# Kernel optimization log

Hardware: AMD Instinct MI355X
Metric: run time of the kernel (lower is better)

Reference implementation:

```python
import jax, jax.numpy as jnp
import numpy as np

NUM_CAMS, BS, NUM_QUERY, MAX_LEN, EMBED_DIMS, NPTS = 6, 1, 40000, 10000, 256, 4


def setup_inputs() -> dict:
    key = jax.random.key(0)
    kq, kr, km = jax.random.split(key, 3)
    query = jax.random.normal(kq, (BS, NUM_QUERY, EMBED_DIMS), dtype=jnp.float32)
    reference_points_cam = jax.random.normal(
        kr, (NUM_CAMS, BS, NUM_QUERY, NPTS, 2), dtype=jnp.float32)
    bev_mask = jax.random.randint(km, (NUM_CAMS, BS, NUM_QUERY, NPTS), 0, 2).astype(jnp.int32)
    return {"query": query, "reference_points_cam": reference_points_cam, "bev_mask": bev_mask}


def reference(query, reference_points_cam, bev_mask):
    # valid[c, q]: query q is seen by camera c (any of the NPTS mask bits set); bs == 1
    valid = (bev_mask > 0).any(-1)            # (cams, bs, Q) bool
    valid0 = valid[:, 0]                      # (cams, Q)

    # Stable stream compaction: valid indices first, in ascending query order.
    order = jnp.argsort(~valid0, axis=-1, stable=True)      # (cams, Q)
    indexes = order[:, :MAX_LEN].astype(jnp.int32)          # (cams, max_len)
    indexes_len = jnp.minimum(valid0.sum(-1), MAX_LEN).astype(jnp.int32)  # (cams,)

    # Padded gather/rebatch; zero out slots beyond each camera's valid count.
    pos_ok = jnp.arange(MAX_LEN)[None, :] < indexes_len[:, None]          # (cams, max_len)
    queries_rebatch = query[0][indexes]                                   # (cams, max_len, E)
    queries_rebatch = jnp.where(pos_ok[:, :, None], queries_rebatch, 0.0)

    ref0 = reference_points_cam[:, 0]                                     # (cams, Q, NPTS, 2)
    reference_points_rebatch = jax.vmap(lambda r, i: r[i])(ref0, indexes) # (cams, max_len, NPTS, 2)
    reference_points_rebatch = jnp.where(
        pos_ok[:, :, None, None], reference_points_rebatch, 0.0)

    # count_norm: 1 / (number of cameras that see each query, clamped to >= 1)
    count = valid.astype(jnp.float32).sum(0)                 # (bs, Q)
    count_norm = (1.0 / jnp.maximum(count, 1.0))[..., None]  # (bs, Q, 1)

    return (indexes,
            indexes_len,
            queries_rebatch.reshape(BS * NUM_CAMS, MAX_LEN, EMBED_DIMS),
            reference_points_rebatch.reshape(BS * NUM_CAMS, MAX_LEN, NPTS, 2),
            count_norm)
```

## Files before the change

### kernel.cpp

```cpp
#include <hip/hip_runtime.h>
#include <hip/hip_bf16.h>

#define NUM_CAMS 6
#define NQ       40000
#define MAX_LEN  10000
#define ED       256
#define NBLK     ((NQ + 255) / 256)

typedef float f32x2 __attribute__((ext_vector_type(2)));

#define OFF_IDX  0
#define OFF_LEN  (NUM_CAMS * MAX_LEN)
#define OFF_Q    (OFF_LEN + NUM_CAMS)
#define OFF_REF  (OFF_Q + NUM_CAMS * MAX_LEN * ED)
#define OFF_CNT  (OFF_REF + NUM_CAMS * MAX_LEN * 8)

#define WS_OFF 0
#define WS_LEN (NUM_CAMS * NBLK)
#define WS_POS (WS_LEN + NUM_CAMS + 4)
#define WS_NEED_BYTES ((WS_POS + NUM_CAMS * NQ) * 4)

#define QBLOCKS      (NQ / 4)
#define TAIL_BLOCKS  (NUM_CAMS * MAX_LEN / 4)
#define CNT_BLOCKS   ((NQ + 255) / 256)
#define GATHER_BLOCKS (NUM_CAMS * MAX_LEN / 4)

__global__ void kA_counts(const int* __restrict__ bev, float* __restrict__ out,
                          int* __restrict__ ws) {
    __shared__ int cnt[NUM_CAMS];
    const int tid = threadIdx.x;
    const int blk = blockIdx.x;
    const int q   = blk * 256 + tid;
    if (tid < NUM_CAMS) cnt[tid] = 0;
    __syncthreads();
    const int lane = tid & 63;
    const bool inb = q < NQ;
    int myCount = 0;
    #pragma unroll
    for (int cam = 0; cam < NUM_CAMS; ++cam) {
        bool v = false;
        if (inb) {
            const int4 m = *reinterpret_cast<const int4*>(bev + ((size_t)cam * NQ + q) * 4);
            v = (m.x > 0) | (m.y > 0) | (m.z > 0) | (m.w > 0);
        }
        myCount += v ? 1 : 0;
        unsigned long long bal = __ballot(v);
        if (lane == 0) atomicAdd(&cnt[cam], __popcll(bal));
    }
    if (inb) out[OFF_CNT + q] = 1.0f / fmaxf((float)myCount, 1.0f);
    __syncthreads();
    if (tid < NUM_CAMS) ws[WS_OFF + tid * NBLK + blk] = cnt[tid];
}

__global__ void kBC_indexes(const int* __restrict__ bev, float* __restrict__ out,
                            int* __restrict__ ws, int usePos) {
    const int blk = blockIdx.x;
    const int cam = blockIdx.y;
    const int tid = threadIdx.x;
    const int lane = tid & 63;
    const int wave = tid >> 6;

    const int part = (tid < NBLK) ? ws[WS_OFF + cam * NBLK + tid] : 0;
    int t = part;
    int o = (tid < blk) ? part : 0;
    #pragma unroll
    for (int d = 1; d < 64; d <<= 1) {
        t += __shfl_xor(t, d, 64);
        o += __shfl_xor(o, d, 64);
    }
    __shared__ int sT[4], sO[4];
    if (lane == 0) { sT[wave] = t; sO[wave] = o; }
    __syncthreads();
    const int total    = sT[0] + sT[1] + sT[2] + sT[3];
    const int blockOff = sO[0] + sO[1] + sO[2] + sO[3];

    if (blk == 0 && tid == 0) {
        const int len = total < MAX_LEN ? total : MAX_LEN;
        ws[WS_LEN + cam] = len;
        out[OFF_LEN + cam] = (float)len;
    }

    const int q   = blk * 256 + tid;
    const bool inb = q < NQ;
    bool v = false;
    if (inb) {
        const int4 m = *reinterpret_cast<const int4*>(bev + ((size_t)cam * NQ + q) * 4);
        v = (m.x > 0) | (m.y > 0) | (m.z > 0) | (m.w > 0);
    }
    const unsigned long long bal = __ballot(v);
    __shared__ int waveSums[4];
    if (lane == 0) waveSums[wave] = __popcll(bal);
    __syncthreads();
    int waveOff = 0;
    #pragma unroll
    for (int w = 0; w < 4; ++w)
        if (w < wave) waveOff += waveSums[w];
    const int prefix = __popcll(bal & ((1ull << lane) - 1ull));
    if (inb) {
        const int vb  = blockOff + waveOff + prefix;
        const int pos = v ? vb : (total + (q - vb));
        if (pos < MAX_LEN) out[OFF_IDX + cam * MAX_LEN + pos] = (float)q;
        if (usePos) ws[WS_POS + cam * NQ + q] = (v && vb < MAX_LEN) ? vb : -1;
    }
}

__global__ void kGatherQ(const float* __restrict__ query, const float* __restrict__ refp,
                         float* __restrict__ out, const int* __restrict__ ws) {
    const int blk   = blockIdx.x;
    const int tid   = threadIdx.x;
    const int group = tid >> 6;
    const int lane  = tid & 63;
    if (blk >= QBLOCKS) {
        const int rowId = (blk - QBLOCKS) * 4 + group;
        const int cam   = rowId / MAX_LEN;
        const int j     = rowId - cam * MAX_LEN;
        if (j < ws[WS_LEN + cam]) return;
        const f32x2 z = (f32x2)(0.f);
        f32x2* o2 = reinterpret_cast<f32x2*>(out + OFF_Q + (size_t)rowId * ED + lane * 4);
        o2[0] = z; o2[1] = z;
        if (lane < 4)
            *reinterpret_cast<f32x2*>(out + OFF_REF + (size_t)rowId * 8 + lane * 2) = z;
        return;
    }
    const int q = blk * 4 + group;

    int pos[NUM_CAMS];
    bool any = false;
    #pragma unroll
    for (int cam = 0; cam < NUM_CAMS; ++cam) {
        const int p = ws[WS_POS + cam * NQ + q];
        pos[cam] = p;
        any |= (p >= 0);
    }
    if (!any) return;

    const float4 vq = *reinterpret_cast<const float4*>(query + (size_t)q * ED + lane * 4);
    f32x2 a; a.x = vq.x; a.y = vq.y;
    f32x2 b; b.x = vq.z; b.y = vq.w;

    #pragma unroll
    for (int cam = 0; cam < NUM_CAMS; ++cam) {
        const int p = pos[cam];
        if (p >= 0) {
            f32x2* o2 = reinterpret_cast<f32x2*>(out + OFF_Q + ((size_t)cam * MAX_LEN + p) * ED + lane * 4);
            o2[0] = a;
            o2[1] = b;
            if (lane < 4) {
                const f32x2 r = *reinterpret_cast<const f32x2*>(refp + ((size_t)cam * NQ + q) * 8 + lane * 2);
                *reinterpret_cast<f32x2*>(out + OFF_REF + ((size_t)cam * MAX_LEN + p) * 8 + lane * 2) = r;
            }
        }
    }
}

__global__ void kGather(const float* __restrict__ query, const float* __restrict__ refp,
                        float* __restrict__ out, const int* __restrict__ ws,
                        const int* __restrict__ bev) {
    const int blk = blockIdx.x;
    const int tid = threadIdx.x;
    if (blk >= GATHER_BLOCKS) {
        const int q = (blk - GATHER_BLOCKS) * 256 + tid;
        if (q < NQ) {
            int cnt = 0;
            #pragma unroll
            for (int cam = 0; cam < NUM_CAMS; ++cam) {
                const int4 m = *reinterpret_cast<const int4*>(bev + ((size_t)cam * NQ + q) * 4);
                cnt += ((m.x > 0) | (m.y > 0) | (m.z > 0) | (m.w > 0)) ? 1 : 0;
            }
            out[OFF_CNT + q] = 1.0f / fmaxf((float)cnt, 1.0f);
        }
        return;
    }
    const int rowId = blk * 4 + (tid >> 6);
    const int lane  = tid & 63;
    const int cam   = rowId / MAX_LEN;
    const int j     = rowId - cam * MAX_LEN;
    const int len   = ws[WS_LEN + cam];

    f32x2 a = (f32x2)(0.f), b = (f32x2)(0.f), r0 = (f32x2)(0.f), r1 = (f32x2)(0.f);
    if (j < len) {
        const int idx = (int)out[OFF_IDX + cam * MAX_LEN + j];
        const float4 vq = *reinterpret_cast<const float4*>(query + (size_t)idx * ED + lane * 4);
        a.x = vq.x; a.y = vq.y;
        b.x = vq.z; b.y = vq.w;
        if (lane < 2) {
            const float4 r = *reinterpret_cast<const float4*>(refp + ((size_t)cam * NQ + idx) * 8 + lane * 4);
            r0.x = r.x; r0.y = r.y;
            r1.x = r.z; r1.y = r.w;
        }
    }
    f32x2* o2 = reinterpret_cast<f32x2*>(out + OFF_Q + (size_t)rowId * ED + lane * 4);
    o2[0] = a;
    o2[1] = b;
    if (lane < 2) {
        f32x2* r2 = reinterpret_cast<f32x2*>(out + OFF_REF + (size_t)rowId * 8 + lane * 4);
        r2[0] = r0;
        r2[1] = r1;
    }
}

extern "C" void kernel_launch(void* const* d_in, const int* in_sizes, int n_in,
                              void* d_out, int out_size, void* d_ws, size_t ws_size,
                              hipStream_t stream) {
    const float* query = (const float*)d_in[0];
    const float* refp  = (const float*)d_in[1];
    const int*   bev   = (const int*)d_in[2];
    float* out = (float*)d_out;
    int*   ws  = (int*)d_ws;
    const int usePos = (ws_size >= (size_t)WS_NEED_BYTES) ? 1 : 0;

    kA_counts<<<NBLK, 256, 0, stream>>>(bev, out, ws);
    kBC_indexes<<<dim3(NBLK, NUM_CAMS), 256, 0, stream>>>(bev, out, ws, usePos);
    if (usePos) {
        kGatherQ<<<QBLOCKS + TAIL_BLOCKS, 256, 0, stream>>>(query, refp, out, ws);
    } else {
        kGather<<<GATHER_BLOCKS + CNT_BLOCKS, 256, 0, stream>>>(query, refp, out, ws, bev);
    }
}
```

Measured before the change: 31.20 us.

## Cache per-wave validity ballots in workspace and use grid-stride gather

The counting kernel now stores each wave's 64-bit validity ballot in workspace, so the index kernel reads one mask per wave instead of reloading the mask tensor and re-ballotting. The gather kernel switches from one block per work item (about 25k blocks) to a fixed 2048-block grid-stride loop. This is meant to cut redundant mask-tensor reads and block launch/scheduling overhead. In exchange it adds workspace writes and makes each block work serially through several items, which may lower memory-level parallelism.

Measured after the change: 30.99 us (median of 2 runs). No clear change (-0.7%).

```diff
diff --git a/kernel.cpp b/kernel.cpp
--- a/kernel.cpp
+++ b/kernel.cpp
@@ -15,18 +15,21 @@
 #define OFF_REF  (OFF_Q + NUM_CAMS * MAX_LEN * ED)
 #define OFF_CNT  (OFF_REF + NUM_CAMS * MAX_LEN * 8)
 
-#define WS_OFF 0
-#define WS_LEN (NUM_CAMS * NBLK)
-#define WS_POS (WS_LEN + NUM_CAMS + 4)
+#define WS_OFF    0
+#define WS_MASK_I 960
+#define WS_MASK_N (NUM_CAMS * NBLK * 4)
+#define WS_LEN    (WS_MASK_I + 2 * WS_MASK_N)
+#define WS_POS    (WS_LEN + 8)
 #define WS_NEED_BYTES ((WS_POS + NUM_CAMS * NQ) * 4)
 
 #define QBLOCKS      (NQ / 4)
 #define TAIL_BLOCKS  (NUM_CAMS * MAX_LEN / 4)
+#define GATHER_GRID  2048
 #define CNT_BLOCKS   ((NQ + 255) / 256)
 #define GATHER_BLOCKS (NUM_CAMS * MAX_LEN / 4)
 
 __global__ void kA_counts(const int* __restrict__ bev, float* __restrict__ out,
-                          int* __restrict__ ws) {
+                          int* __restrict__ ws, int usePos) {
     __shared__ int cnt[NUM_CAMS];
     const int tid = threadIdx.x;
     const int blk = blockIdx.x;
@@ -34,7 +37,9 @@
     if (tid < NUM_CAMS) cnt[tid] = 0;
     __syncthreads();
     const int lane = tid & 63;
+    const int wave = tid >> 6;
     const bool inb = q < NQ;
+    unsigned long long* wsm = reinterpret_cast<unsigned long long*>(ws + WS_MASK_I);
     int myCount = 0;
     #pragma unroll
     for (int cam = 0; cam < NUM_CAMS; ++cam) {
@@ -44,8 +49,11 @@
             v = (m.x > 0) | (m.y > 0) | (m.z > 0) | (m.w > 0);
         }
         myCount += v ? 1 : 0;
-        unsigned long long bal = __ballot(v);
-        if (lane == 0) atomicAdd(&cnt[cam], __popcll(bal));
+        const unsigned long long bal = __ballot(v);
+        if (lane == 0) {
+            atomicAdd(&cnt[cam], __popcll(bal));
+            if (usePos) wsm[((size_t)cam * NBLK + blk) * 4 + wave] = bal;
+        }
     }
     if (inb) out[OFF_CNT + q] = 1.0f / fmaxf((float)myCount, 1.0f);
     __syncthreads();
@@ -68,8 +76,23 @@
         t += __shfl_xor(t, d, 64);
         o += __shfl_xor(o, d, 64);
     }
-    __shared__ int sT[4], sO[4];
-    if (lane == 0) { sT[wave] = t; sO[wave] = o; }
+    __shared__ int sT[4], sO[4], waveSums[4];
+
+    unsigned long long mask;
+    if (usePos) {
+        const unsigned long long* wsm =
+            reinterpret_cast<const unsigned long long*>(ws + WS_MASK_I);
+        mask = wsm[((size_t)cam * NBLK + blk) * 4 + wave];
+    } else {
+        const int q = blk * 256 + tid;
+        bool v = false;
+        if (q < NQ) {
+            const int4 m = *reinterpret_cast<const int4*>(bev + ((size_t)cam * NQ + q) * 4);
+            v = (m.x > 0) | (m.y > 0) | (m.z > 0) | (m.w > 0);
+        }
+        mask = __ballot(v);
+    }
+    if (lane == 0) { sT[wave] = t; sO[wave] = o; waveSums[wave] = __popcll(mask); }
     __syncthreads();
     const int total    = sT[0] + sT[1] + sT[2] + sT[3];
     const int blockOff = sO[0] + sO[1] + sO[2] + sO[3];
@@ -80,23 +103,14 @@
         out[OFF_LEN + cam] = (float)len;
     }
 
-    const int q   = blk * 256 + tid;
-    const bool inb = q < NQ;
-    bool v = false;
-    if (inb) {
-        const int4 m = *reinterpret_cast<const int4*>(bev + ((size_t)cam * NQ + q) * 4);
-        v = (m.x > 0) | (m.y > 0) | (m.z > 0) | (m.w > 0);
-    }
-    const unsigned long long bal = __ballot(v);
-    __shared__ int waveSums[4];
-    if (lane == 0) waveSums[wave] = __popcll(bal);
-    __syncthreads();
-    int waveOff = 0;
-    #pragma unroll
-    for (int w = 0; w < 4; ++w)
-        if (w < wave) waveOff += waveSums[w];
-    const int prefix = __popcll(bal & ((1ull << lane) - 1ull));
-    if (inb) {
+    const int q = blk * 256 + tid;
+    if (q < NQ) {
+        int waveOff = 0;
+        #pragma unroll
+        for (int w = 0; w < 4; ++w)
+            if (w < wave) waveOff += waveSums[w];
+        const bool v     = (mask >> lane) & 1ull;
+        const int prefix = __popcll(mask & ((1ull << lane) - 1ull));
         const int vb  = blockOff + waveOff + prefix;
         const int pos = v ? vb : (total + (q - vb));
         if (pos < MAX_LEN) out[OFF_IDX + cam * MAX_LEN + pos] = (float)q;
@@ -106,49 +120,49 @@
 
 __global__ void kGatherQ(const float* __restrict__ query, const float* __restrict__ refp,
                          float* __restrict__ out, const int* __restrict__ ws) {
-    const int blk   = blockIdx.x;
     const int tid   = threadIdx.x;
     const int group = tid >> 6;
     const int lane  = tid & 63;
-    if (blk >= QBLOCKS) {
-        const int rowId = (blk - QBLOCKS) * 4 + group;
-        const int cam   = rowId / MAX_LEN;
-        const int j     = rowId - cam * MAX_LEN;
-        if (j < ws[WS_LEN + cam]) return;
-        const f32x2 z = (f32x2)(0.f);
-        f32x2* o2 = reinterpret_cast<f32x2*>(out + OFF_Q + (size_t)rowId * ED + lane * 4);
-        o2[0] = z; o2[1] = z;
-        if (lane < 4)
-            *reinterpret_cast<f32x2*>(out + OFF_REF + (size_t)rowId * 8 + lane * 2) = z;
-        return;
-    }
-    const int q = blk * 4 + group;
-
-    int pos[NUM_CAMS];
-    bool any = false;
-    #pragma unroll
-    for (int cam = 0; cam < NUM_CAMS; ++cam) {
-        const int p = ws[WS_POS + cam * NQ + q];
-        pos[cam] = p;
-        any |= (p >= 0);
-    }
-    if (!any) return;
-
-    const float4 vq = *reinterpret_cast<const float4*>(query + (size_t)q * ED + lane * 4);
-    f32x2 a; a.x = vq.x; a.y = vq.y;
-    f32x2 b; b.x = vq.z; b.y = vq.w;
-
-    #pragma unroll
-    for (int cam = 0; cam < NUM_CAMS; ++cam) {
-        const int p = pos[cam];
-        if (p >= 0) {
-            f32x2* o2 = reinterpret_cast<f32x2*>(out + OFF_Q + ((size_t)cam * MAX_LEN + p) * ED + lane * 4);
-            o2[0] = a;
-            o2[1] = b;
-            if (lane < 4) {
-                const f32x2 r = *reinterpret_cast<const f32x2*>(refp + ((size_t)cam * NQ + q) * 8 + lane * 2);
-                *reinterpret_cast<f32x2*>(out + OFF_REF + ((size_t)cam * MAX_LEN + p) * 8 + lane * 2) = r;
+    for (int item = blockIdx.x; item < QBLOCKS + TAIL_BLOCKS; item += gridDim.x) {
+        if (item < QBLOCKS) {
+            const int q = item * 4 + group;
+            int pos[NUM_CAMS];
+            bool any = false;
+            #pragma unroll
+            for (int cam = 0; cam < NUM_CAMS; ++cam) {
+                const int p = ws[WS_POS + cam * NQ + q];
+                pos[cam] = p;
+                any |= (p >= 0);
             }
+            if (!any) continue;
+
+            const float4 vq = *reinterpret_cast<const float4*>(query + (size_t)q * ED + lane * 4);
+            f32x2 a; a.x = vq.x; a.y = vq.y;
+            f32x2 b; b.x = vq.z; b.y = vq.w;
+
+            #pragma unroll
+            for (int cam = 0; cam < NUM_CAMS; ++cam) {
+                const int p = pos[cam];
+                if (p >= 0) {
+                    f32x2* o2 = reinterpret_cast<f32x2*>(out + OFF_Q + ((size_t)cam * MAX_LEN + p) * ED + lane * 4);
+                    o2[0] = a;
+                    o2[1] = b;
+                    if (lane < 4) {
+                        const f32x2 r = *reinterpret_cast<const f32x2*>(refp + ((size_t)cam * NQ + q) * 8 + lane * 2);
+                        *reinterpret_cast<f32x2*>(out + OFF_REF + ((size_t)cam * MAX_LEN + p) * 8 + lane * 2) = r;
+                    }
+                }
+            }
+        } else {
+            const int rowId = (item - QBLOCKS) * 4 + group;
+            const int cam   = rowId / MAX_LEN;
+            const int j     = rowId - cam * MAX_LEN;
+            if (j < ws[WS_LEN + cam]) continue;
+            const f32x2 z = (f32x2)(0.f);
+            f32x2* o2 = reinterpret_cast<f32x2*>(out + OFF_Q + (size_t)rowId * ED + lane * 4);
+            o2[0] = z; o2[1] = z;
+            if (lane < 4)
+                *reinterpret_cast<f32x2*>(out + OFF_REF + (size_t)rowId * 8 + lane * 2) = z;
         }
     }
 }
@@ -209,10 +223,10 @@
     int*   ws  = (int*)d_ws;
     const int usePos = (ws_size >= (size_t)WS_NEED_BYTES) ? 1 : 0;
 
-    kA_counts<<<NBLK, 256, 0, stream>>>(bev, out, ws);
+    kA_counts<<<NBLK, 256, 0, stream>>>(bev, out, ws, usePos);
     kBC_indexes<<<dim3(NBLK, NUM_CAMS), 256, 0, stream>>>(bev, out, ws, usePos);
     if (usePos) {
-        kGatherQ<<<QBLOCKS + TAIL_BLOCKS, 256, 0, stream>>>(query, refp, out, ws);
+        kGatherQ<<<GATHER_GRID, 256, 0, stream>>>(query, refp, out, ws);
     } else {
         kGather<<<GATHER_BLOCKS + CNT_BLOCKS, 256, 0, stream>>>(query, refp, out, ws, bev);
     }
```
